# Kernel tuning notes

Measured on AMD Instinct MI355X. Metric: run time of the kernel, lower is better.

Reference implementation:

```python
import jax, jax.numpy as jnp
import numpy as np

D = 1024
H = 16
HD = D // H
EPS = 1e-5


def layer_norm(x, g, b):
    mu = jnp.mean(x, axis=-1, keepdims=True)
    var = jnp.mean((x - mu) ** 2, axis=-1, keepdims=True)
    return (x - mu) * jax.lax.rsqrt(var + EPS) * g + b


def setup_inputs() -> dict:
    key = jax.random.key(0)
    ks = jax.random.split(key, 10)
    s = lambda fan_in: 1.0 / np.sqrt(fan_in)
    inp = {
        "x": jax.random.normal(ks[0], (2, 2048, D), dtype=jnp.float32),
        "w_qkv": jax.random.uniform(ks[1], (D, 3 * D), minval=-s(D), maxval=s(D)),
        "b_qkv": jnp.zeros((3 * D,), jnp.float32),
        "w_fc": jax.random.uniform(ks[2], (D, D), minval=-s(D), maxval=s(D)),
        "b_fc": jnp.zeros((D,), jnp.float32),
        "ln1_g": jnp.ones((D,), jnp.float32),
        "ln1_b": jnp.zeros((D,), jnp.float32),
        "ln2_g": jnp.ones((D,), jnp.float32),
        "ln2_b": jnp.zeros((D,), jnp.float32),
        "w1": jax.random.uniform(ks[3], (D, 4 * D), minval=-s(D), maxval=s(D)),
        "b1": jnp.zeros((4 * D,), jnp.float32),
        "w2": jax.random.uniform(ks[4], (4 * D, D), minval=-s(4 * D), maxval=s(4 * D)),
        "b2": jnp.zeros((D,), jnp.float32),
    }
    return inp


def reference(x, w_qkv, b_qkv, w_fc, b_fc, ln1_g, ln1_b, ln2_g, ln2_b, w1, b1, w2, b2):
    B, T, C = x.shape
    # --- attention sublayer (pre-norm) ---
    h = layer_norm(x, ln1_g, ln1_b)
    qkv = (h @ w_qkv + b_qkv).reshape(B, T, 3, H, HD)
    q, k, v = qkv[:, :, 0], qkv[:, :, 1], qkv[:, :, 2]  # [B,T,H,HD]
    scores = jnp.einsum("bqhd,bkhd->bhqk", q, k) / np.sqrt(HD).astype(np.float32)
    causal = jnp.tril(jnp.ones((T, T), dtype=bool))
    scores = jnp.where(causal, scores, -jnp.inf)
    weights = jax.nn.softmax(scores, axis=-1)
    out = jnp.einsum("bhqk,bkhd->bqhd", weights, v).reshape(B, T, C)
    x = x + out @ w_fc + b_fc
    # --- MLP sublayer (pre-norm) ---
    h = layer_norm(x, ln2_g, ln2_b)
    h = jax.nn.gelu(h @ w1 + b1, approximate=False) @ w2 + b2
    return x + h
```

## Files before the change

kernel.cpp:

```cpp
#include <hip/hip_runtime.h>
#include <hip/hip_bf16.h>
#include <cstdint>
#include <cstddef>

#define SEQ 2048
#define DM  1024

typedef __attribute__((ext_vector_type(8))) __bf16 bf16x8;
typedef __attribute__((ext_vector_type(4))) float  f32x4;
using bf16 = __hip_bfloat16;

__device__ __forceinline__ void gload_lds16(const bf16* g, bf16* l) {
  __builtin_amdgcn_global_load_lds((const __attribute__((address_space(1))) void*)g,
                                   (__attribute__((address_space(3))) void*)l,
                                   16, 0, 0);
}
__device__ __forceinline__ void wb4() { asm volatile("s_waitcnt vmcnt(4)\n\ts_barrier" ::: "memory"); }
__device__ __forceinline__ void wb0() { asm volatile("s_waitcnt vmcnt(0)\n\ts_barrier" ::: "memory"); }

__global__ void transpose_to_bf16(const float* __restrict__ in, bf16* __restrict__ out,
                                  int K, int N) {
  __shared__ float tile[32][33];
  const int k0 = blockIdx.y * 32, n0 = blockIdx.x * 32;
  const int tx = threadIdx.x, ty = threadIdx.y;
#pragma unroll
  for (int i = ty; i < 32; i += 8)
    tile[i][tx] = in[(size_t)(k0 + i) * N + n0 + tx];
  __syncthreads();
#pragma unroll
  for (int i = ty; i < 32; i += 8)
    out[(size_t)(n0 + i) * K + k0 + tx] = __float2bfloat16(tile[tx][i]);
}

__global__ void ln_to_bf16(const float* __restrict__ x, const float* __restrict__ g,
                           const float* __restrict__ bt, bf16* __restrict__ out) {
  const int row = blockIdx.x;
  const float4 v = ((const float4*)(x + (size_t)row * DM))[threadIdx.x];
  float s  = v.x + v.y + v.z + v.w;
  float s2 = v.x * v.x + v.y * v.y + v.z * v.z + v.w * v.w;
#pragma unroll
  for (int o = 32; o > 0; o >>= 1) { s += __shfl_down(s, o); s2 += __shfl_down(s2, o); }
  __shared__ float red[8];
  const int wave = threadIdx.x >> 6, lane = threadIdx.x & 63;
  if (lane == 0) { red[wave] = s; red[4 + wave] = s2; }
  __syncthreads();
  s  = red[0] + red[1] + red[2] + red[3];
  s2 = red[4] + red[5] + red[6] + red[7];
  const float mu  = s * (1.f / DM);
  const float var = s2 * (1.f / DM) - mu * mu;
  const float r   = rsqrtf(var + 1e-5f);
  const float4 gv = ((const float4*)g)[threadIdx.x];
  const float4 bv = ((const float4*)bt)[threadIdx.x];
  bf16* o = out + (size_t)row * DM + threadIdx.x * 4;
  o[0] = __float2bfloat16((v.x - mu) * r * gv.x + bv.x);
  o[1] = __float2bfloat16((v.y - mu) * r * gv.y + bv.y);
  o[2] = __float2bfloat16((v.z - mu) * r * gv.z + bv.z);
  o[3] = __float2bfloat16((v.w - mu) * r * gv.w + bv.w);
}

enum { EP_BF16 = 0, EP_GELU = 1, EP_RESID = 2, EP_QKV = 3 };

template <int MODE>
__global__ __launch_bounds__(512, 2)
void gemm256(const bf16* __restrict__ A, const bf16* __restrict__ Bt,
             const float* __restrict__ bias,
             bf16* __restrict__ Cb, bf16* __restrict__ vt,
             int M, int N, int K) {
  constexpr int ATILE = 256 * 64;
  constexpr int BTILE = 128 * 64;
  __shared__ __attribute__((aligned(16))) bf16 As[3 * ATILE];
  __shared__ __attribute__((aligned(16))) bf16 Bs[2 * BTILE];
  const int tid = threadIdx.x;
  const int w = tid >> 6, lane = tid & 63;
  const int l16 = lane & 15, lq = lane >> 4;
  const int m0 = blockIdx.x * 256, n0 = blockIdx.y * 128;
  const int wr = (w >> 1) * 64, wc = (w & 1) * 64;

  f32x4 acc[4][4];
#pragma unroll
  for (int i = 0; i < 4; i++)
#pragma unroll
    for (int j = 0; j < 4; j++) acc[i][j] = 0;

  const int srow = tid >> 3;
  const int scb  = (tid & 7) ^ (srow & 7);
  const bf16* gA = A  + (size_t)(m0 + srow) * K + scb * 8;
  const bf16* gB = Bt + (size_t)(n0 + srow) * K + scb * 8;
  const int lw = w * 512;

  auto stageA = [&](int t) {
    const int kt = t << 6;
    bf16* d = As + (t % 3) * ATILE + lw;
#pragma unroll
    for (int i = 0; i < 4; i++)
      gload_lds16(gA + (size_t)i * 64 * K + kt, d + i * 4096);
  };
  auto stageB = [&](int t) {
    const int kt = t << 6;
    bf16* d = Bs + (t & 1) * BTILE + lw;
#pragma unroll
    for (int j = 0; j < 2; j++)
      gload_lds16(gB + (size_t)j * 64 * K + kt, d + j * 4096);
  };

  const int NKT = K >> 6;
  stageB(0); stageA(0); stageA(1);

  const int sxa = l16 & 7;
  for (int it = 0; it < NKT; ++it) {
    if (it + 1 < NKT) wb4(); else wb0();
    if (it + 1 < NKT) stageB(it + 1);
    if (it + 2 < NKT) stageA(it + 2);
    const bf16* a  = As + (it % 3) * ATILE;
    const bf16* bb = Bs + (it & 1) * BTILE;
#pragma unroll
    for (int ks = 0; ks < 2; ks++) {
      bf16x8 af[4], bfv[4];
#pragma unroll
      for (int mi = 0; mi < 4; mi++) {
        const int row = wr + mi * 16 + l16;
        af[mi] = *(const bf16x8*)(a + row * 64 + (((ks * 4 + lq) ^ sxa) << 3));
      }
#pragma unroll
      for (int ni = 0; ni < 4; ni++) {
        const int row = wc + ni * 16 + l16;
        bfv[ni] = *(const bf16x8*)(bb + row * 64 + (((ks * 4 + lq) ^ sxa) << 3));
      }
      __builtin_amdgcn_s_setprio(1);
#pragma unroll
      for (int mi = 0; mi < 4; mi++)
#pragma unroll
        for (int ni = 0; ni < 4; ni++)
          acc[mi][ni] = __builtin_amdgcn_mfma_f32_16x16x32_bf16(af[mi], bfv[ni], acc[mi][ni], 0, 0, 0);
      __builtin_amdgcn_s_setprio(0);
    }
  }

#pragma unroll
  for (int ni = 0; ni < 4; ni++) {
    const int col = n0 + wc + ni * 16 + l16;
    const float bb = bias[col];
#pragma unroll
    for (int mi = 0; mi < 4; mi++) {
      if constexpr (MODE == EP_QKV) {
        const int row0 = m0 + wr + mi * 16 + lq * 4;
        if (col >= 2048) {
          __attribute__((aligned(8))) bf16 pk[4];
#pragma unroll
          for (int r = 0; r < 4; r++) pk[r] = __float2bfloat16(acc[mi][ni][r] + bb);
          *(uint2*)(vt + (size_t)((row0 >> 11) * 1024 + (col - 2048)) * SEQ + (row0 & 2047)) =
              *(const uint2*)pk;
        } else {
#pragma unroll
          for (int r = 0; r < 4; r++)
            Cb[(size_t)(row0 + r) * N + col] = __float2bfloat16(acc[mi][ni][r] + bb);
        }
      } else {
#pragma unroll
        for (int r = 0; r < 4; r++) {
          const int row = m0 + wr + mi * 16 + lq * 4 + r;
          float v = acc[mi][ni][r] + bb;
          v = 0.5f * v * (1.0f + erff(v * 0.70710678118654752f));
          Cb[(size_t)row * N + col] = __float2bfloat16(v);
        }
      }
    }
  }
}

__global__ __launch_bounds__(256, 4)
void gemm_bt64(const bf16* __restrict__ A, const bf16* __restrict__ Bt,
               const float* __restrict__ bias, const float* __restrict__ resid,
               float* __restrict__ Cf, int M, int N, int K) {
  constexpr int TILE = 64 * 64;
  __shared__ __attribute__((aligned(16))) bf16 As[2 * TILE];
  __shared__ __attribute__((aligned(16))) bf16 Bs[2 * TILE];
  const int tid  = threadIdx.x;
  const int wave = tid >> 6, lane = tid & 63;
  const int l16 = lane & 15, lq = lane >> 4;
  const int m0 = blockIdx.x * 64, n0 = blockIdx.y * 64;
  const int wr = (wave >> 1) * 32, wc = (wave & 1) * 32;

  f32x4 acc[2][2];
#pragma unroll
  for (int i = 0; i < 2; i++)
#pragma unroll
    for (int j = 0; j < 2; j++) acc[i][j] = 0;

  const int srow = tid >> 3;
  const int scb  = (tid & 7) ^ (srow & 7);
  const bf16* ga0 = A  + (size_t)(m0 + srow) * K + scb * 8;
  const bf16* ga1 = A  + (size_t)(m0 + srow + 32) * K + scb * 8;
  const bf16* gb0 = Bt + (size_t)(n0 + srow) * K + scb * 8;
  const bf16* gb1 = Bt + (size_t)(n0 + srow + 32) * K + scb * 8;
  const int ld0 = wave * 512;
  const int ld1 = 2048 + wave * 512;

  gload_lds16(ga0, As + ld0);
  gload_lds16(ga1, As + ld1);
  gload_lds16(gb0, Bs + ld0);
  gload_lds16(gb1, Bs + ld1);

  const int sxa = l16 & 7;

  const int NKT = K >> 6;
  for (int it = 0; it < NKT; ++it) {
    __syncthreads();
    const int cur = (it & 1) * TILE;
    if (it + 1 < NKT) {
      const int nxt = ((it + 1) & 1) * TILE;
      const int kt = (it + 1) << 6;
      gload_lds16(ga0 + kt, As + nxt + ld0);
      gload_lds16(ga1 + kt, As + nxt + ld1);
      gload_lds16(gb0 + kt, Bs + nxt + ld0);
      gload_lds16(gb1 + kt, Bs + nxt + ld1);
    }
    bf16x8 af[2][2], bfv[2][2];
#pragma unroll
    for (int mi = 0; mi < 2; mi++) {
      const int row = wr + mi * 16 + l16;
#pragma unroll
      for (int kk = 0; kk < 2; kk++)
        af[mi][kk] = *(const bf16x8*)(As + cur + row * 64 + (((kk * 4 + lq) ^ sxa) << 3));
    }
#pragma unroll
    for (int ni = 0; ni < 2; ni++) {
      const int row = wc + ni * 16 + l16;
#pragma unroll
      for (int kk = 0; kk < 2; kk++)
        bfv[ni][kk] = *(const bf16x8*)(Bs + cur + row * 64 + (((kk * 4 + lq) ^ sxa) << 3));
    }
#pragma unroll
    for (int kk = 0; kk < 2; kk++)
#pragma unroll
      for (int mi = 0; mi < 2; mi++)
#pragma unroll
        for (int ni = 0; ni < 2; ni++)
          acc[mi][ni] = __builtin_amdgcn_mfma_f32_16x16x32_bf16(af[mi][kk], bfv[ni][kk],
                                                                acc[mi][ni], 0, 0, 0);
  }

#pragma unroll
  for (int ni = 0; ni < 2; ni++) {
    const int col = n0 + wc + ni * 16 + l16;
    const float bb = bias[col];
#pragma unroll
    for (int mi = 0; mi < 2; mi++) {
#pragma unroll
      for (int r = 0; r < 4; r++) {
        const int row = m0 + wr + mi * 16 + lq * 4 + r;
        const size_t idx = (size_t)row * N + col;
        Cf[idx] = resid[idx] + acc[mi][ni][r] + bb;
      }
    }
  }
}

#define SCALE_LOG2 0.18033688011112042f

__global__ __launch_bounds__(512, 2)
void flash_attn(const bf16* __restrict__ qkv, const bf16* __restrict__ VTg,
                bf16* __restrict__ out) {
  const int idx  = blockIdx.x;
  const int praw = idx & 15;
  const int p    = ((idx >> 8) & 1) ? (15 - praw) : praw;
  const int bh   = (idx >> 4) & 31;
  const int h    = bh & 15;
  const int b    = bh >> 4;
  const int qlow = p, qhigh = 31 - p;

  const int tid = threadIdx.x;
  const int w = tid >> 6, lane = tid & 63;
  const int wq = w & 3, hf = w >> 2;
  const int l16 = lane & 15, lq = lane >> 4;
  const int myqb = hf ? qlow : qhigh;

  const size_t base = (size_t)b * SEQ * 3072;
  const bf16* Qg = qkv + base + (size_t)h * 64;
  const bf16* Kg = qkv + base + 1024 + (size_t)h * 64;
  const bf16* Vt = VTg + (size_t)(b * 1024 + h * 64) * SEQ;

  __shared__ __attribute__((aligned(16))) bf16 Ks[2 * 4096];
  __shared__ __attribute__((aligned(16))) bf16 VTs[2 * 4096];
  __shared__ __attribute__((aligned(16))) bf16 Ps[8 * 1024];

  const int srow = tid >> 3;
  const int scb  = (tid & 7) ^ (srow & 7);
  const bf16* gK = Kg + (size_t)srow * 3072 + scb * 8;
  const bf16* gV = Vt + (size_t)srow * SEQ + scb * 8;
  const int ldst = w * 512;

  gload_lds16(gK, Ks + ldst);
  gload_lds16(gV, VTs + ldst);

  const bf16* qrow = Qg + (size_t)(myqb * 64 + wq * 16 + l16) * 3072 + lq * 8;
  const bf16x8 qf0 = *(const bf16x8*)(qrow);
  const bf16x8 qf1 = *(const bf16x8*)(qrow + 32);

  const int koffA = l16 * 64 + ((lq ^ (l16 & 7)) << 3);
  const int koffB = l16 * 64 + (((4 + lq) ^ (l16 & 7)) << 3);
  const int l16h = l16 >> 3;
  const int pco  = w * 1024 + (l16 & 7);

  f32x4 oacc[4];
#pragma unroll
  for (int i = 0; i < 4; i++) oacc[i] = 0;
  float lsum[4] = {0.f, 0.f, 0.f, 0.f};

  const int nkt = qhigh + 1;
  for (int kb = 0; kb < nkt; ++kb) {
    __syncthreads();
    const int cur = (kb & 1) * 4096;
    if (kb + 1 < nkt) {
      const int nxt = ((kb + 1) & 1) * 4096;
      const size_t ko = (size_t)(kb + 1) * 64;
      gload_lds16(gK + ko * 3072, Ks + nxt + ldst);
      gload_lds16(gV + ko, VTs + nxt + ldst);
    }

    if (kb <= myqb) {
      f32x4 sacc[4];
#pragma unroll
      for (int nt = 0; nt < 4; nt++) sacc[nt] = 0;
#pragma unroll
      for (int nt = 0; nt < 4; nt++) {
        const bf16x8 kf0 = *(const bf16x8*)(Ks + cur + nt * 1024 + koffA);
        const bf16x8 kf1 = *(const bf16x8*)(Ks + cur + nt * 1024 + koffB);
        sacc[nt] = __builtin_amdgcn_mfma_f32_16x16x32_bf16(qf0, kf0, sacc[nt], 0, 0, 0);
        sacc[nt] = __builtin_amdgcn_mfma_f32_16x16x32_bf16(qf1, kf1, sacc[nt], 0, 0, 0);
      }

      if (kb == myqb) {
#pragma unroll
        for (int r = 0; r < 4; r++) {
          const int rowp = lq * 4 + r;
          const int qloc = wq * 16 + rowp;
          float e[4];
#pragma unroll
          for (int nt = 0; nt < 4; nt++) {
            float sv = sacc[nt][r] * SCALE_LOG2;
            sv = fminf(sv, 88.f);
            if (nt * 16 + l16 > qloc) sv = -1e30f;
            e[nt] = exp2f(sv);
            Ps[pco + rowp * 64 + ((((nt * 2 + l16h)) ^ (rowp & 7)) << 3)] = __float2bfloat16(e[nt]);
          }
          lsum[r] += (e[0] + e[1]) + (e[2] + e[3]);
        }
      } else {
#pragma unroll
        for (int r = 0; r < 4; r++) {
          const int rowp = lq * 4 + r;
          float e[4];
#pragma unroll
          for (int nt = 0; nt < 4; nt++) {
            float sv = sacc[nt][r] * SCALE_LOG2;
            sv = fminf(sv, 88.f);
            e[nt] = exp2f(sv);
            Ps[pco + rowp * 64 + ((((nt * 2 + l16h)) ^ (rowp & 7)) << 3)] = __float2bfloat16(e[nt]);
          }
          lsum[r] += (e[0] + e[1]) + (e[2] + e[3]);
        }
      }

      const bf16x8 pf0 = *(const bf16x8*)(Ps + w * 1024 + koffA);
      const bf16x8 pf1 = *(const bf16x8*)(Ps + w * 1024 + koffB);
#pragma unroll
      for (int dt = 0; dt < 4; dt++) {
        const bf16x8 vf0 = *(const bf16x8*)(VTs + cur + dt * 1024 + koffA);
        const bf16x8 vf1 = *(const bf16x8*)(VTs + cur + dt * 1024 + koffB);
        oacc[dt] = __builtin_amdgcn_mfma_f32_16x16x32_bf16(pf0, vf0, oacc[dt], 0, 0, 0);
        oacc[dt] = __builtin_amdgcn_mfma_f32_16x16x32_bf16(pf1, vf1, oacc[dt], 0, 0, 0);
      }
    }
  }

#pragma unroll
  for (int r = 0; r < 4; r++) {
    float l = lsum[r];
    l += __shfl_xor(l, 1);
    l += __shfl_xor(l, 2);
    l += __shfl_xor(l, 4);
    l += __shfl_xor(l, 8);
    lsum[r] = 1.f / l;
  }
#pragma unroll
  for (int dt = 0; dt < 4; dt++)
#pragma unroll
    for (int r = 0; r < 4; r++) {
      const int qrow_ = myqb * 64 + wq * 16 + lq * 4 + r;
      const float v = oacc[dt][r] * lsum[r];
      out[(size_t)(b * SEQ + qrow_) * DM + h * 64 + dt * 16 + l16] = __float2bfloat16(v);
    }
}

extern "C" void kernel_launch(void* const* d_in, const int* in_sizes, int n_in,
                              void* d_out, int out_size, void* d_ws, size_t ws_size,
                              hipStream_t stream) {
  const float* x     = (const float*)d_in[0];
  const float* w_qkv = (const float*)d_in[1];
  const float* b_qkv = (const float*)d_in[2];
  const float* w_fc  = (const float*)d_in[3];
  const float* b_fc  = (const float*)d_in[4];
  const float* ln1_g = (const float*)d_in[5];
  const float* ln1_b = (const float*)d_in[6];
  const float* ln2_g = (const float*)d_in[7];
  const float* ln2_b = (const float*)d_in[8];
  const float* w1    = (const float*)d_in[9];
  const float* b1    = (const float*)d_in[10];
  const float* w2    = (const float*)d_in[11];
  const float* b2    = (const float*)d_in[12];
  float* out = (float*)d_out;

  char* ws    = (char*)d_ws;
  float* x2   = (float*)(ws);
  bf16* VTg   = (bf16*)(ws);
  bf16* big   = (bf16*)(ws + (size_t)(16 << 20));
  bf16* small = (bf16*)(ws + (size_t)(48 << 20));
  bf16* wT    = (bf16*)(ws + (size_t)(56 << 20));

  const dim3 tb(32, 8);

  ln_to_bf16<<<dim3(4096), dim3(256), 0, stream>>>(x, ln1_g, ln1_b, small);
  transpose_to_bf16<<<dim3(96, 32), tb, 0, stream>>>(w_qkv, wT, 1024, 3072);
  gemm256<EP_QKV><<<dim3(16, 24), dim3(512), 0, stream>>>(
      small, wT, b_qkv, big, VTg, 4096, 3072, 1024);
  flash_attn<<<dim3(512), dim3(512), 0, stream>>>(big, VTg, small);
  transpose_to_bf16<<<dim3(32, 32), tb, 0, stream>>>(w_fc, wT, 1024, 1024);
  gemm_bt64<<<dim3(64, 16), dim3(256), 0, stream>>>(
      small, wT, b_fc, x, x2, 4096, 1024, 1024);
  ln_to_bf16<<<dim3(4096), dim3(256), 0, stream>>>(x2, ln2_g, ln2_b, small);
  transpose_to_bf16<<<dim3(128, 32), tb, 0, stream>>>(w1, wT, 1024, 4096);
  gemm256<EP_GELU><<<dim3(16, 32), dim3(512), 0, stream>>>(
      small, wT, b1, big, nullptr, 4096, 4096, 1024);
  transpose_to_bf16<<<dim3(32, 128), tb, 0, stream>>>(w2, wT, 4096, 1024);
  gemm_bt64<<<dim3(64, 16), dim3(256), 0, stream>>>(
      big, wT, b2, x2, out, 4096, 1024, 4096);
}
```

Measured before the change: 376.2 us.

## Restructure big GEMMs with triple-buffered phased pipeline and XCD-aware tile remapping

Rewrites the 256x128 GEMM to keep a unified triple-buffered LDS stage for A and B. The global-to-LDS loads for stage g+2 are now spread across four compute phases with barriers between them, and the wave layout changes to 2x4 with 128x32 per-wave tiles. Adds a workgroup remap that groups tiles into 4x4 supertiles per XCD chiplet for better L2 reuse, and applies the same remap to the 64x64 GEMM. The extra barriers per phase and higher LDS use may reduce overlap or occupancy.

```diff
diff --git a/kernel.cpp b/kernel.cpp
--- a/kernel.cpp
+++ b/kernel.cpp
@@ -15,8 +15,17 @@
                                    (__attribute__((address_space(3))) void*)l,
                                    16, 0, 0);
 }
-__device__ __forceinline__ void wb4() { asm volatile("s_waitcnt vmcnt(4)\n\ts_barrier" ::: "memory"); }
-__device__ __forceinline__ void wb0() { asm volatile("s_waitcnt vmcnt(0)\n\ts_barrier" ::: "memory"); }
+
+template <int GM, int GN>
+__device__ __forceinline__ void remap_wg(int id, int& bm, int& bn) {
+  constexpr int NWG = GM * GN;
+  constexpr int CPX = NWG / 8;
+  id = (id & 7) * CPX + (id >> 3);
+  const int st = id >> 4, wi = id & 15;
+  constexpr int STM = GM / 4;
+  bm = (st % STM) * 4 + (wi & 3);
+  bn = (st / STM) * 4 + (wi >> 2);
+}
 
 __global__ void transpose_to_bf16(const float* __restrict__ in, bf16* __restrict__ out,
                                   int K, int N) {
@@ -60,114 +69,125 @@
 
 enum { EP_BF16 = 0, EP_GELU = 1, EP_RESID = 2, EP_QKV = 3 };
 
-template <int MODE>
+template <int MODE, int GM, int GN>
 __global__ __launch_bounds__(512, 2)
-void gemm256(const bf16* __restrict__ A, const bf16* __restrict__ Bt,
-             const float* __restrict__ bias,
-             bf16* __restrict__ Cb, bf16* __restrict__ vt,
-             int M, int N, int K) {
-  constexpr int ATILE = 256 * 64;
-  constexpr int BTILE = 128 * 64;
-  __shared__ __attribute__((aligned(16))) bf16 As[3 * ATILE];
-  __shared__ __attribute__((aligned(16))) bf16 Bs[2 * BTILE];
+void gemm_fat(const bf16* __restrict__ A, const bf16* __restrict__ Bt,
+              const float* __restrict__ bias,
+              bf16* __restrict__ Cb, bf16* __restrict__ vt,
+              int M, int N, int K) {
+  constexpr int ASZ = 256 * 64;
+  constexpr int BSZ = 128 * 64;
+  constexpr int TSZ = ASZ + BSZ;
+  __shared__ __attribute__((aligned(16))) bf16 lds[3 * TSZ];
   const int tid = threadIdx.x;
   const int w = tid >> 6, lane = tid & 63;
   const int l16 = lane & 15, lq = lane >> 4;
-  const int m0 = blockIdx.x * 256, n0 = blockIdx.y * 128;
-  const int wr = (w >> 1) * 64, wc = (w & 1) * 64;
-
-  f32x4 acc[4][4];
-#pragma unroll
-  for (int i = 0; i < 4; i++)
-#pragma unroll
-    for (int j = 0; j < 4; j++) acc[i][j] = 0;
+  const int wm = w >> 2, wn = w & 3;
+  int bm, bn;
+  remap_wg<GM, GN>(blockIdx.x, bm, bn);
+  const int m0 = bm * 256, n0 = bn * 128;
+
+  f32x4 acc[8][2];
+#pragma unroll
+  for (int i = 0; i < 8; i++)
+#pragma unroll
+    for (int j = 0; j < 2; j++) acc[i][j] = 0;
 
   const int srow = tid >> 3;
   const int scb  = (tid & 7) ^ (srow & 7);
   const bf16* gA = A  + (size_t)(m0 + srow) * K + scb * 8;
   const bf16* gB = Bt + (size_t)(n0 + srow) * K + scb * 8;
-  const int lw = w * 512;
-
-  auto stageA = [&](int t) {
-    const int kt = t << 6;
-    bf16* d = As + (t % 3) * ATILE + lw;
-#pragma unroll
-    for (int i = 0; i < 4; i++)
-      gload_lds16(gA + (size_t)i * 64 * K + kt, d + i * 4096);
+  const int dw = w * 512;
+
+  auto stA = [&](int t, int j) {
+    gload_lds16(gA + (size_t)(j * 64) * K + (t << 6),
+                lds + (t % 3) * TSZ + j * 4096 + dw);
   };
-  auto stageB = [&](int t) {
-    const int kt = t << 6;
-    bf16* d = Bs + (t & 1) * BTILE + lw;
-#pragma unroll
-    for (int j = 0; j < 2; j++)
-      gload_lds16(gB + (size_t)j * 64 * K + kt, d + j * 4096);
+  auto stB = [&](int t, int j) {
+    gload_lds16(gB + (size_t)(j * 64) * K + (t << 6),
+                lds + (t % 3) * TSZ + ASZ + j * 4096 + dw);
   };
 
   const int NKT = K >> 6;
-  stageB(0); stageA(0); stageA(1);
-
-  const int sxa = l16 & 7;
-  for (int it = 0; it < NKT; ++it) {
-    if (it + 1 < NKT) wb4(); else wb0();
-    if (it + 1 < NKT) stageB(it + 1);
-    if (it + 2 < NKT) stageA(it + 2);
-    const bf16* a  = As + (it % 3) * ATILE;
-    const bf16* bb = Bs + (it & 1) * BTILE;
-#pragma unroll
-    for (int ks = 0; ks < 2; ks++) {
-      bf16x8 af[4], bfv[4];
+  stA(0, 0); stA(0, 1); stA(0, 2); stA(0, 3); stB(0, 0); stB(0, 1);
+  stA(1, 0); stA(1, 1); stA(1, 2); stA(1, 3); stB(1, 0); stB(1, 1);
+
+  const int sx = l16 & 7;
+  for (int g = 0; g < NKT; ++g) {
+    if (g + 1 < NKT) asm volatile("s_waitcnt vmcnt(6)" ::: "memory");
+    else             asm volatile("s_waitcnt vmcnt(0)" ::: "memory");
+    __builtin_amdgcn_s_barrier();
+    const bf16* buf  = lds + (g % 3) * TSZ;
+    const bf16* bufB = buf + ASZ;
+    const bool st = (g + 2 < NKT);
+#pragma unroll
+    for (int ph = 0; ph < 4; ++ph) {
+      const int rh = ph >> 1, ks = ph & 1;
+      bf16x8 af[4], bv[2];
 #pragma unroll
       for (int mi = 0; mi < 4; mi++) {
-        const int row = wr + mi * 16 + l16;
-        af[mi] = *(const bf16x8*)(a + row * 64 + (((ks * 4 + lq) ^ sxa) << 3));
-      }
-#pragma unroll
-      for (int ni = 0; ni < 4; ni++) {
-        const int row = wc + ni * 16 + l16;
-        bfv[ni] = *(const bf16x8*)(bb + row * 64 + (((ks * 4 + lq) ^ sxa) << 3));
-      }
+        const int row = wm * 128 + rh * 64 + mi * 16 + l16;
+        af[mi] = *(const bf16x8*)(buf + row * 64 + (((ks * 4 + lq) ^ sx) << 3));
+      }
+#pragma unroll
+      for (int nj = 0; nj < 2; nj++) {
+        const int row = wn * 32 + nj * 16 + l16;
+        bv[nj] = *(const bf16x8*)(bufB + row * 64 + (((ks * 4 + lq) ^ sx) << 3));
+      }
+      if (st) {
+        if (ph == 0)      { stA(g + 2, 0); stA(g + 2, 1); }
+        else if (ph == 1) { stA(g + 2, 2); stA(g + 2, 3); }
+        else if (ph == 2) { stB(g + 2, 0); stB(g + 2, 1); }
+      }
+      __builtin_amdgcn_s_barrier();
+      asm volatile("s_waitcnt lgkmcnt(0)" ::: "memory");
       __builtin_amdgcn_s_setprio(1);
 #pragma unroll
       for (int mi = 0; mi < 4; mi++)
 #pragma unroll
-        for (int ni = 0; ni < 4; ni++)
-          acc[mi][ni] = __builtin_amdgcn_mfma_f32_16x16x32_bf16(af[mi], bfv[ni], acc[mi][ni], 0, 0, 0);
+        for (int nj = 0; nj < 2; nj++)
+          acc[rh * 4 + mi][nj] = __builtin_amdgcn_mfma_f32_16x16x32_bf16(
+              af[mi], bv[nj], acc[rh * 4 + mi][nj], 0, 0, 0);
       __builtin_amdgcn_s_setprio(0);
-    }
-  }
-
-#pragma unroll
-  for (int ni = 0; ni < 4; ni++) {
-    const int col = n0 + wc + ni * 16 + l16;
-    const float bb = bias[col];
-#pragma unroll
-    for (int mi = 0; mi < 4; mi++) {
-      if constexpr (MODE == EP_QKV) {
-        const int row0 = m0 + wr + mi * 16 + lq * 4;
-        if (col >= 2048) {
-          __attribute__((aligned(8))) bf16 pk[4];
-#pragma unroll
-          for (int r = 0; r < 4; r++) pk[r] = __float2bfloat16(acc[mi][ni][r] + bb);
-          *(uint2*)(vt + (size_t)((row0 >> 11) * 1024 + (col - 2048)) * SEQ + (row0 & 2047)) =
-              *(const uint2*)pk;
-        } else {
-#pragma unroll
-          for (int r = 0; r < 4; r++)
-            Cb[(size_t)(row0 + r) * N + col] = __float2bfloat16(acc[mi][ni][r] + bb);
+      __builtin_amdgcn_s_barrier();
+    }
+  }
+
+  if (MODE == EP_QKV && n0 >= 2048) {
+#pragma unroll
+    for (int nj = 0; nj < 2; nj++) {
+      const int col = n0 + wn * 32 + nj * 16 + l16;
+      const float bb = bias[col];
+#pragma unroll
+      for (int mi = 0; mi < 8; mi++) {
+        const int row0 = m0 + wm * 128 + (mi >> 2) * 64 + (mi & 3) * 16 + lq * 4;
+        __attribute__((aligned(8))) bf16 pk[4];
+#pragma unroll
+        for (int r = 0; r < 4; r++) pk[r] = __float2bfloat16(acc[mi][nj][r] + bb);
+        *(uint2*)(vt + (size_t)((row0 >> 11) * 1024 + (col - 2048)) * SEQ + (row0 & 2047)) =
+            *(const uint2*)pk;
+      }
+    }
+  } else {
+#pragma unroll
+    for (int nj = 0; nj < 2; nj++) {
+      const int col = n0 + wn * 32 + nj * 16 + l16;
+      const float bb = bias[col];
+#pragma unroll
+      for (int mi = 0; mi < 8; mi++) {
+        const int rowb = m0 + wm * 128 + (mi >> 2) * 64 + (mi & 3) * 16 + lq * 4;
+#pragma unroll
+        for (int r = 0; r < 4; r++) {
+          float v = acc[mi][nj][r] + bb;
+          if (MODE == EP_GELU) v = 0.5f * v * (1.0f + erff(v * 0.70710678118654752f));
+          Cb[(size_t)(rowb + r) * N + col] = __float2bfloat16(v);
         }
-      } else {
-#pragma unroll
-        for (int r = 0; r < 4; r++) {
-          const int row = m0 + wr + mi * 16 + lq * 4 + r;
-          float v = acc[mi][ni][r] + bb;
-          v = 0.5f * v * (1.0f + erff(v * 0.70710678118654752f));
-          Cb[(size_t)row * N + col] = __float2bfloat16(v);
-        }
-      }
-    }
-  }
-}
-
+      }
+    }
+  }
+}
+
+template <int GM, int GN>
 __global__ __launch_bounds__(256, 4)
 void gemm_bt64(const bf16* __restrict__ A, const bf16* __restrict__ Bt,
                const float* __restrict__ bias, const float* __restrict__ resid,
@@ -178,7 +198,9 @@
   const int tid  = threadIdx.x;
   const int wave = tid >> 6, lane = tid & 63;
   const int l16 = lane & 15, lq = lane >> 4;
-  const int m0 = blockIdx.x * 64, n0 = blockIdx.y * 64;
+  int bm, bn;
+  remap_wg<GM, GN>(blockIdx.x, bm, bn);
+  const int m0 = bm * 64, n0 = bn * 64;
   const int wr = (wave >> 1) * 32, wc = (wave & 1) * 32;
 
   f32x4 acc[2][2];
@@ -422,17 +444,17 @@
 
   ln_to_bf16<<<dim3(4096), dim3(256), 0, stream>>>(x, ln1_g, ln1_b, small);
   transpose_to_bf16<<<dim3(96, 32), tb, 0, stream>>>(w_qkv, wT, 1024, 3072);
-  gemm256<EP_QKV><<<dim3(16, 24), dim3(512), 0, stream>>>(
+  gemm_fat<EP_QKV, 16, 24><<<dim3(384), dim3(512), 0, stream>>>(
       small, wT, b_qkv, big, VTg, 4096, 3072, 1024);
   flash_attn<<<dim3(512), dim3(512), 0, stream>>>(big, VTg, small);
   transpose_to_bf16<<<dim3(32, 32), tb, 0, stream>>>(w_fc, wT, 1024, 1024);
-  gemm_bt64<<<dim3(64, 16), dim3(256), 0, stream>>>(
+  gemm_bt64<64, 16><<<dim3(1024), dim3(256), 0, stream>>>(
       small, wT, b_fc, x, x2, 4096, 1024, 1024);
   ln_to_bf16<<<dim3(4096), dim3(256), 0, stream>>>(x2, ln2_g, ln2_b, small);
   transpose_to_bf16<<<dim3(128, 32), tb, 0, stream>>>(w1, wT, 1024, 4096);
-  gemm256<EP_GELU><<<dim3(16, 32), dim3(512), 0, stream>>>(
+  gemm_fat<EP_GELU, 16, 32><<<dim3(512), dim3(512), 0, stream>>>(
       small, wT, b1, big, nullptr, 4096, 4096, 1024);
   transpose_to_bf16<<<dim3(32, 128), tb, 0, stream>>>(w2, wT, 4096, 1024);
-  gemm_bt64<<<dim3(64, 16), dim3(256), 0, stream>>>(
+  gemm_bt64<64, 16><<<dim3(1024), dim3(256), 0, stream>>>(
       big, wT, b2, x2, out, 4096, 1024, 4096);
 }
```

Measured after the change: 371.8 us. About the same (-1.2%).
